# Optimization experiments

Measured on AMD Instinct MI355X. Metric: run time of the kernel, lower is better.

The kernel has to match this reference:

```python
import jax, jax.numpy as jnp
import numpy as np

B, T, E = 4, 2048, 2048
H, HKV, HD = 16, 8, 128
THETA = 10000.0
SCALE_BASE = 512.0


def _rotate_half(x):
    x1, x2 = jnp.split(x, 2, axis=-1)
    return jnp.concatenate([-x2, x1], axis=-1)


def _xpos_tables(seqlen):
    # cos/sin/scale tables for XPos rotary, all [seqlen, HD], fp32 compute dtype
    half_idx = jnp.arange(0, HD, 2, dtype=jnp.float32)
    inv_freq = 1.0 / (THETA ** (half_idx / HD))            # [HD/2]
    t = jnp.arange(seqlen, dtype=jnp.float32)
    freqs = jnp.outer(t, inv_freq)                          # [seqlen, HD/2]
    emb = jnp.concatenate([freqs, freqs], axis=-1)          # [seqlen, HD]
    cos, sin = jnp.cos(emb), jnp.sin(emb)
    # xpos decay: ((2i + 0.4d)/(1.4d)) ** ((t - L/2)/scale_base)
    scale_vec = (half_idx + 0.4 * HD) / (1.4 * HD)          # [HD/2]
    power = (t - seqlen // 2) / SCALE_BASE                  # [seqlen]
    scale = scale_vec[None, :] ** power[:, None]            # [seqlen, HD/2]
    scale = jnp.concatenate([scale, scale], axis=-1)        # [seqlen, HD]
    return cos, sin, scale


def setup_inputs() -> dict:
    key = jax.random.key(0)
    ks = jax.random.split(key, 5)
    std = 0.02
    return {
        "x": jax.random.normal(ks[0], (B, T, E), dtype=jnp.float32),
        "W_q": jax.random.normal(ks[1], (E, H * HD), dtype=jnp.float32) * std,
        "W_k": jax.random.normal(ks[2], (E, HKV * HD), dtype=jnp.float32) * std,
        "W_v": jax.random.normal(ks[3], (E, HKV * HD), dtype=jnp.float32) * std,
        "W_o": jax.random.normal(ks[4], (E, E), dtype=jnp.float32) * std,
    }


def reference(x, W_q, W_k, W_v, W_o):
    b, t, _ = x.shape
    q = (x @ W_q).reshape(b, t, H, HD)       # [B,T,H,HD]
    k = (x @ W_k).reshape(b, t, HKV, HD)     # [B,T,HKV,HD]
    v = (x @ W_v).reshape(b, t, HKV, HD)
    rep = H // HKV                            # GQA: repeat_interleave over head dim
    k = jnp.repeat(k, rep, axis=2)
    v = jnp.repeat(v, rep, axis=2)

    cos, sin, scale = _xpos_tables(t)         # past_len = 0 (no kv cache)
    cos = cos[None, :, None, :]
    sin = sin[None, :, None, :]
    scale = scale[None, :, None, :]
    q = q * scale
    q = q * cos + _rotate_half(q) * sin
    k = k / scale
    k = k * cos + _rotate_half(k) * sin

    inv_sqrt_d = 1.0 / jnp.sqrt(jnp.float32(HD))
    scores = jnp.einsum('bqhd,bkhd->bhqk', q, k) * inv_sqrt_d  # [B,H,T,T]
    causal = jnp.triu(jnp.ones((t, t), dtype=bool), k=1)
    scores = jnp.where(causal[None, None], -jnp.inf, scores)
    probs = jax.nn.softmax(scores, axis=-1)
    attn = jnp.einsum('bhqk,bkhd->bqhd', probs, v)             # [B,T,H,HD]
    out = attn.reshape(b, t, E) @ W_o
    return out
```

## Files before the change

### kernel.cpp

```cpp
#include <hip/hip_runtime.h>

typedef _Float16 f16;
typedef __attribute__((ext_vector_type(8))) _Float16 f16x8;
typedef __attribute__((ext_vector_type(4))) _Float16 f16x4;
typedef __attribute__((ext_vector_type(4))) float f32x4;
typedef __attribute__((ext_vector_type(16))) float f32x16;
typedef __attribute__((ext_vector_type(4))) unsigned u32x4;

#define T_SEQ 2048
#define NBATCH 4

__device__ __forceinline__ void gld_lds16(const f16* g, f16* l) {
    __builtin_amdgcn_global_load_lds((const __attribute__((address_space(1))) void*)g,
                                     (__attribute__((address_space(3))) void*)l, 16, 0, 0);
}

__device__ __forceinline__ unsigned pk2(float a, float b) {
    __attribute__((ext_vector_type(2))) __fp16 h = __builtin_amdgcn_cvt_pkrtz(a, b);
    return __builtin_bit_cast(unsigned, h);
}

__global__ __launch_bounds__(256) void k_cast(const float* __restrict__ in,
                                              f16* __restrict__ out, int n4) {
    int i = blockIdx.x * 256 + threadIdx.x;
    if (i < n4) {
        float4 v = ((const float4*)in)[i];
        f16x4 o = { (f16)v.x, (f16)v.y, (f16)v.z, (f16)v.w };
        ((f16x4*)out)[i] = o;
    }
}

__global__ __launch_bounds__(256) void k_transpose(const float* __restrict__ src,
                                                   f16* __restrict__ dst, int K, int N) {
    __shared__ float tile[32][33];
    int n0 = blockIdx.x * 32, k0 = blockIdx.y * 32;
    int tx = threadIdx.x & 31, ty = threadIdx.x >> 5;
#pragma unroll
    for (int j = 0; j < 32; j += 8)
        tile[ty + j][tx] = src[(size_t)(k0 + ty + j) * N + n0 + tx];
    __syncthreads();
#pragma unroll
    for (int j = 0; j < 32; j += 8)
        dst[(size_t)(n0 + ty + j) * K + k0 + tx] = (f16)tile[tx][ty + j];
}

__global__ __launch_bounds__(256) void k_tables(float* __restrict__ tab) {
    int i = blockIdx.x * 256 + threadIdx.x;
    int t = i >> 6, f = i & 63;
    float inv_freq = powf(10000.0f, -(2.0f * f) / 128.0f);
    float ang = (float)t * inv_freq;
    float sv = (2.0f * f + 51.2f) / 179.2f;
    float pw = ((float)t - 1024.0f) / 512.0f;
    tab[i] = cosf(ang);
    tab[131072 + i] = sinf(ang);
    tab[262144 + i] = powf(sv, pw);
}

__global__ __launch_bounds__(256) void k_vtrans(const f16* __restrict__ qkv, f16* __restrict__ vtg) {
    const int kt = blockIdx.x, bk = blockIdx.y;
    const int b = bk >> 3, kvh = bk & 7;
    const int tid = threadIdx.x;
    __shared__ f16 tile[64][132];
#pragma unroll
    for (int p = 0; p < 4; ++p) {
        int idx = p * 256 + tid;
        int r = idx >> 4, dc = (idx & 15) * 8;
        f16x8 v = *(const f16x8*)(qkv + (size_t)(b * T_SEQ + kt * 64 + r) * 4096 + 3072 + kvh * 128 + dc);
#pragma unroll
        for (int j = 0; j < 8; ++j) tile[r][dc + j] = v[j];
    }
    __syncthreads();
    f16* outb = vtg + (size_t)(bk * 32 + kt) * 8192;
#pragma unroll
    for (int p = 0; p < 4; ++p) {
        int c = p * 256 + tid;
        int kchunk = c >> 7, d = c & 127;
        f16x8 o;
#pragma unroll
        for (int j = 0; j < 8; ++j) o[j] = tile[kchunk * 8 + j][d];
        *(f16x8*)(outb + (size_t)c * 8) = o;
    }
}

template <typename OutT>
__global__ __launch_bounds__(512, 1) void k_gemm256(const f16* __restrict__ A,
                                                    const f16* __restrict__ B,
                                                    OutT* __restrict__ C, int M, int N, int K) {
    extern __shared__ char smem[];
    f16* As = (f16*)smem;
    f16* Bs = (f16*)smem + 32768;
    const int tid = threadIdx.x, lane = tid & 63, w = tid >> 6;
    const int wr4 = w >> 1, wc2 = w & 1;
    const int cq = lane & 15, gq = lane >> 4;
    const int nbx = gridDim.x;
    const int nwg = nbx * gridDim.y;
    const int bid0 = blockIdx.y * nbx + blockIdx.x;
    const int bid = (bid0 & 7) * (nwg >> 3) + (bid0 >> 3);
    const int m0 = (bid / nbx) * 256, n0 = (bid % nbx) * 256;
    const int KT = K >> 6;

    f32x4 acc[2][2][2][4] = {};
    f16x8 aL[2][2], aH[2][2], bL[4][2], bH[4][2];

    auto stageA = [&](int buf, int half, int t) {
#pragma unroll
        for (int r = 0; r < 2; ++r) {
            int cb = r * 512 + w * 64;
            int c = cb + lane;
            int row = c >> 3, cc = c & 7;
            gld_lds16(A + (size_t)(m0 + half * 128 + row) * K + t * 64 + ((cc ^ (row & 7)) * 8),
                      As + buf * 16384 + half * 8192 + cb * 8);
        }
    };
    auto stageB = [&](int buf, int half, int t) {
#pragma unroll
        for (int r = 0; r < 2; ++r) {
            int cb = r * 512 + w * 64;
            int c = cb + lane;
            int row = c >> 3, cc = c & 7;
            gld_lds16(B + (size_t)(n0 + half * 128 + row) * K + t * 64 + ((cc ^ (row & 7)) * 8),
                      Bs + buf * 16384 + half * 8192 + cb * 8);
        }
    };
    auto rdA = [&](int buf, int qr, f16x8 a[2][2]) {
#pragma unroll
        for (int mi = 0; mi < 2; ++mi)
#pragma unroll
            for (int ks = 0; ks < 2; ++ks) {
                int R = qr * 128 + wr4 * 32 + mi * 16 + cq;
                a[mi][ks] = *(const f16x8*)&As[buf * 16384 + R * 64 + (((ks * 4 + gq) ^ (cq & 7)) * 8)];
            }
    };
    auto rdB = [&](int buf, int qc, f16x8 b[4][2]) {
#pragma unroll
        for (int ni = 0; ni < 4; ++ni)
#pragma unroll
            for (int ks = 0; ks < 2; ++ks) {
                int R = qc * 128 + wc2 * 64 + ni * 16 + cq;
                b[ni][ks] = *(const f16x8*)&Bs[buf * 16384 + R * 64 + (((ks * 4 + gq) ^ (cq & 7)) * 8)];
            }
    };

    stageA(0, 0, 0); stageB(0, 0, 0); stageB(0, 1, 0); stageA(0, 1, 0);
    if (KT > 1) { stageA(1, 0, 1); stageB(1, 0, 1); stageB(1, 1, 1); }
    asm volatile("s_waitcnt vmcnt(6)");
    __builtin_amdgcn_s_barrier();

#pragma unroll 1
    for (int t = 0; t < KT; ++t) {
        const int buf = t & 1;
        rdA(buf, 0, aL); rdB(buf, 0, bL);
        if (t + 1 < KT) stageA(buf ^ 1, 1, t + 1);
        __builtin_amdgcn_s_barrier();
        asm volatile("s_waitcnt lgkmcnt(0)");
        __builtin_amdgcn_sched_barrier(0);
        __builtin_amdgcn_s_setprio(1);
#pragma unroll
        for (int mi = 0; mi < 2; ++mi)
#pragma unroll
            for (int ni = 0; ni < 4; ++ni)
#pragma unroll
                for (int ks = 0; ks < 2; ++ks)
                    acc[0][0][mi][ni] = __builtin_amdgcn_mfma_f32_16x16x32_f16(aL[mi][ks], bL[ni][ks], acc[0][0][mi][ni], 0, 0, 0);
        __builtin_amdgcn_s_setprio(0);
        __builtin_amdgcn_s_barrier();
        rdB(buf, 1, bH);
        if (t + 2 < KT) stageA(buf, 0, t + 2);
        __builtin_amdgcn_s_barrier();
        asm volatile("s_waitcnt lgkmcnt(0)");
        __builtin_amdgcn_sched_barrier(0);
        __builtin_amdgcn_s_setprio(1);
#pragma unroll
        for (int mi = 0; mi < 2; ++mi)
#pragma unroll
            for (int ni = 0; ni < 4; ++ni)
#pragma unroll
                for (int ks = 0; ks < 2; ++ks)
                    acc[0][1][mi][ni] = __builtin_amdgcn_mfma_f32_16x16x32_f16(aL[mi][ks], bH[ni][ks], acc[0][1][mi][ni], 0, 0, 0);
        __builtin_amdgcn_s_setprio(0);
        __builtin_amdgcn_s_barrier();
        rdA(buf, 1, aH);
        if (t + 2 < KT) stageB(buf, 0, t + 2);
        __builtin_amdgcn_s_barrier();
        asm volatile("s_waitcnt lgkmcnt(0)");
        __builtin_amdgcn_sched_barrier(0);
        __builtin_amdgcn_s_setprio(1);
#pragma unroll
        for (int mi = 0; mi < 2; ++mi)
#pragma unroll
            for (int ni = 0; ni < 4; ++ni)
#pragma unroll
                for (int ks = 0; ks < 2; ++ks)
                    acc[1][1][mi][ni] = __builtin_amdgcn_mfma_f32_16x16x32_f16(aH[mi][ks], bH[ni][ks], acc[1][1][mi][ni], 0, 0, 0);
        __builtin_amdgcn_s_setprio(0);
        __builtin_amdgcn_s_barrier();
        if (t + 2 < KT) stageB(buf, 1, t + 2);
        __builtin_amdgcn_s_barrier();
        __builtin_amdgcn_sched_barrier(0);
        __builtin_amdgcn_s_setprio(1);
#pragma unroll
        for (int mi = 0; mi < 2; ++mi)
#pragma unroll
            for (int ni = 0; ni < 4; ++ni)
#pragma unroll
                for (int ks = 0; ks < 2; ++ks)
                    acc[1][0][mi][ni] = __builtin_amdgcn_mfma_f32_16x16x32_f16(aH[mi][ks], bL[ni][ks], acc[1][0][mi][ni], 0, 0, 0);
        __builtin_amdgcn_s_setprio(0);
        if (t + 2 < KT) asm volatile("s_waitcnt vmcnt(6)");
        else            asm volatile("s_waitcnt vmcnt(0)");
        __builtin_amdgcn_s_barrier();
    }

#pragma unroll
    for (int qr = 0; qr < 2; ++qr)
#pragma unroll
        for (int qc = 0; qc < 2; ++qc)
#pragma unroll
            for (int mi = 0; mi < 2; ++mi)
#pragma unroll
                for (int ni = 0; ni < 4; ++ni)
#pragma unroll
                    for (int i = 0; i < 4; ++i) {
                        int row = m0 + qr * 128 + wr4 * 32 + mi * 16 + gq * 4 + i;
                        int col = n0 + qc * 128 + wc2 * 64 + ni * 16 + cq;
                        C[(size_t)row * N + col] = (OutT)acc[qr][qc][mi][ni][i];
                    }
}

__global__ __launch_bounds__(256) void k_rope(f16* __restrict__ qkv, const float* __restrict__ tab) {
    int idx = blockIdx.x * 256 + threadIdx.x;
    const int QTOT = NBATCH * T_SEQ * 16 * 64;
    int f, col0, bt;
    bool isQ = idx < QTOT;
    if (isQ) {
        f = idx & 63; int hh = (idx >> 6) & 15; bt = idx >> 10;
        col0 = hh * 128 + f;
    } else {
        int j = idx - QTOT;
        f = j & 63; int hh = (j >> 6) & 7; bt = j >> 9;
        col0 = 2048 + hh * 128 + f;
    }
    int t = bt & (T_SEQ - 1);
    float cs = tab[t * 64 + f], sn = tab[131072 + t * 64 + f], sc = tab[262144 + t * 64 + f];
    float mult = isQ ? sc * 0.08838834764831845f : 1.0f / sc;
    size_t p = (size_t)bt * 4096 + col0;
    float x1 = (float)qkv[p], x2 = (float)qkv[p + 64];
    qkv[p]      = (f16)((x1 * cs - x2 * sn) * mult);
    qkv[p + 64] = (f16)((x2 * cs + x1 * sn) * mult);
}

__global__ __launch_bounds__(256) void k_attn(const f16* __restrict__ qkv,
                                              const f16* __restrict__ vtg,
                                              f16* __restrict__ ao) {
    const int bid0 = blockIdx.x;
    const int bid = (bid0 & 7) * 64 + (bid0 >> 3);
    const int pr = bid & 7, h = (bid >> 3) & 15, b = bid >> 7;
    const int kvh = h >> 1, bk = b * 8 + kvh;
    const int tid = threadIdx.x, lane = tid & 63, w = tid >> 6;
    const int l31 = lane & 31, hi = lane >> 5;

    __shared__ f16 Klds[2][64 * 128];
    __shared__ f16 Vlds[2][8 * 128 * 8];

    const f16* kbase = qkv + (size_t)b * T_SEQ * 4096 + 2048 + kvh * 128;
    const f16* vbase = vtg + (size_t)bk * 32 * 8192;

    auto stage = [&](int buf, int kt) {
#pragma unroll
        for (int qq = 0; qq < 4; ++qq) {
            int c = w * 256 + qq * 64 + lane;
            int row = c >> 4;
            int ch = (c & 15) ^ (row & 15);
            gld_lds16(kbase + (size_t)(kt * 64 + row) * 4096 + ch * 8,
                      &Klds[buf][(w * 256 + qq * 64) * 8]);
        }
#pragma unroll
        for (int qq = 0; qq < 4; ++qq) {
            int c = w * 256 + qq * 64 + lane;
            gld_lds16(vbase + ((size_t)kt * 1024 + c) * 8,
                      &Vlds[buf][(w * 256 + qq * 64) * 8]);
        }
    };

#pragma unroll 1
    for (int hf = 0; hf < 2; ++hf) {
        const int qt = hf ? pr : (15 - pr);
        const int q0 = qt * 128;
        const int nkt = 2 * qt + 2;
        const int qrow = q0 + w * 32 + l31;

        f16x8 qf[8];
#pragma unroll
        for (int ds = 0; ds < 8; ++ds)
            qf[ds] = *(const f16x8*)(qkv + (size_t)(b * T_SEQ + qrow) * 4096 + h * 128 + ds * 16 + hi * 8);

        f32x16 Ot[4] = {};
        float mrow = -1e30f, lrow = 0.0f;

        stage(0, 0);
        __syncthreads();

#pragma unroll 1
        for (int kt = 0; kt < nkt; ++kt) {
            const int kb = kt & 1;
            if (kt + 1 < nkt) stage(kb ^ 1, kt + 1);

            if (!(kt == 2 * qt + 1 && w < 2)) {
                f32x16 St0 = {}, St1 = {};
                __builtin_amdgcn_s_setprio(1);
#pragma unroll
                for (int ds = 0; ds < 8; ++ds) {
                    int slot = (((2 * ds + hi) ^ (l31 & 15)) << 3);
                    f16x8 k0 = *(const f16x8*)&Klds[kb][l31 * 128 + slot];
                    f16x8 k1 = *(const f16x8*)&Klds[kb][(32 + l31) * 128 + slot];
                    St0 = __builtin_amdgcn_mfma_f32_32x32x16_f16(k0, qf[ds], St0, 0, 0, 0);
                    St1 = __builtin_amdgcn_mfma_f32_32x32x16_f16(k1, qf[ds], St1, 0, 0, 0);
                }
                __builtin_amdgcn_s_setprio(0);

                if (kt >= 2 * qt) {
                    int kbase2 = kt * 64;
#pragma unroll
                    for (int r = 0; r < 16; ++r) {
                        int krel = (r & 3) + 8 * (r >> 2) + 4 * hi;
                        if (kbase2 + krel > qrow) St0[r] = -1e30f;
                        if (kbase2 + 32 + krel > qrow) St1[r] = -1e30f;
                    }
                }

                float tm[16];
#pragma unroll
                for (int r = 0; r < 16; ++r) tm[r] = fmaxf(St0[r], St1[r]);
#pragma unroll
                for (int d = 8; d >= 1; d >>= 1)
#pragma unroll
                    for (int r = 0; r < 8; ++r)
                        if (r < d) tm[r] = fmaxf(tm[r], tm[r + d]);
                float tmax = tm[0];
                float mtile = fmaxf(tmax, __shfl_xor(tmax, 32, 64));

                if (!__all((mtile - mrow) <= 8.0f)) {
                    float mnew = fmaxf(mrow, mtile);
                    float fs = __expf(mrow - mnew);
                    mrow = mnew;
                    lrow *= fs;
#pragma unroll
                    for (int dblk = 0; dblk < 4; ++dblk)
#pragma unroll
                        for (int e = 0; e < 16; ++e) Ot[dblk][e] *= fs;
                }
#pragma unroll
                for (int r = 0; r < 16; ++r) {
                    St0[r] = __expf(St0[r] - mrow);
                    St1[r] = __expf(St1[r] - mrow);
                }
                float ts[16];
#pragma unroll
                for (int r = 0; r < 16; ++r) ts[r] = St0[r] + St1[r];
#pragma unroll
                for (int d = 8; d >= 1; d >>= 1)
#pragma unroll
                    for (int r = 0; r < 8; ++r)
                        if (r < d) ts[r] += ts[r + d];
                float tsum = ts[0];
                lrow += tsum + __shfl_xor(tsum, 32, 64);

#define PV_P(o, pos) ((o) < 4 ? St0[((o) & 3) * 4 + (pos)] : St1[((o) & 3) * 4 + (pos)])
#pragma unroll
                for (int s = 0; s < 4; ++s) {
                    unsigned x1 = pk2(PV_P(2 * s, 0), PV_P(2 * s, 1));
                    unsigned x2 = pk2(PV_P(2 * s, 2), PV_P(2 * s, 3));
                    unsigned y1 = pk2(PV_P(2 * s + 1, 0), PV_P(2 * s + 1, 1));
                    unsigned y2 = pk2(PV_P(2 * s + 1, 2), PV_P(2 * s + 1, 3));
                    unsigned sx1 = __shfl_xor(x1, 32, 64);
                    unsigned sx2 = __shfl_xor(x2, 32, 64);
                    unsigned sy1 = __shfl_xor(y1, 32, 64);
                    unsigned sy2 = __shfl_xor(y2, 32, 64);
                    u32x4 pw;
                    pw[0] = hi ? sy1 : x1;
                    pw[1] = hi ? sy2 : x2;
                    pw[2] = hi ? y1 : sx1;
                    pw[3] = hi ? y2 : sx2;
                    f16x8 pa = __builtin_bit_cast(f16x8, pw);
                    __builtin_amdgcn_s_setprio(1);
#pragma unroll
                    for (int dblk = 0; dblk < 4; ++dblk) {
                        f16x8 vb = *(const f16x8*)&Vlds[kb][(((2 * s + hi) << 7) + 32 * dblk + l31) << 3];
                        Ot[dblk] = __builtin_amdgcn_mfma_f32_32x32x16_f16(vb, pa, Ot[dblk], 0, 0, 0);
                    }
                    __builtin_amdgcn_s_setprio(0);
                }
#undef PV_P
            }
            __syncthreads();
        }

        {
            float inv = 1.0f / lrow;
            size_t rowb = (size_t)(b * T_SEQ + qrow) * 2048 + h * 128;
#pragma unroll
            for (int dblk = 0; dblk < 4; ++dblk)
#pragma unroll
                for (int rg = 0; rg < 4; ++rg) {
                    f16x4 o4 = { (f16)(Ot[dblk][rg * 4 + 0] * inv), (f16)(Ot[dblk][rg * 4 + 1] * inv),
                                 (f16)(Ot[dblk][rg * 4 + 2] * inv), (f16)(Ot[dblk][rg * 4 + 3] * inv) };
                    *(f16x4*)(ao + rowb + dblk * 32 + rg * 8 + hi * 4) = o4;
                }
        }
    }
}

extern "C" void kernel_launch(void* const* d_in, const int* in_sizes, int n_in,
                              void* d_out, int out_size, void* d_ws, size_t ws_size,
                              hipStream_t stream) {
    const float* x  = (const float*)d_in[0];
    const float* Wq = (const float*)d_in[1];
    const float* Wk = (const float*)d_in[2];
    const float* Wv = (const float*)d_in[3];
    const float* Wo = (const float*)d_in[4];
    float* out = (float*)d_out;

    f16* xh    = (f16*)d_ws;
    f16* wqkvT = xh + (size_t)16777216;
    f16* woT   = wqkvT + (size_t)8388608;
    f16* qkv   = woT + (size_t)4194304;
    float* tab = (float*)(qkv + (size_t)33554432);
    f16* ao  = xh;
    f16* vtg = wqkvT;

    hipFuncSetAttribute(reinterpret_cast<const void*>(&k_gemm256<f16>),
                        hipFuncAttributeMaxDynamicSharedMemorySize, 131072);
    hipFuncSetAttribute(reinterpret_cast<const void*>(&k_gemm256<float>),
                        hipFuncAttributeMaxDynamicSharedMemorySize, 131072);

    k_cast<<<16384, 256, 0, stream>>>(x, xh, 4194304);
    k_transpose<<<dim3(64, 64), 256, 0, stream>>>(Wq, wqkvT, 2048, 2048);
    k_transpose<<<dim3(32, 64), 256, 0, stream>>>(Wk, wqkvT + (size_t)2048 * 2048, 2048, 1024);
    k_transpose<<<dim3(32, 64), 256, 0, stream>>>(Wv, wqkvT + (size_t)3072 * 2048, 2048, 1024);
    k_transpose<<<dim3(64, 64), 256, 0, stream>>>(Wo, woT, 2048, 2048);
    k_tables<<<512, 256, 0, stream>>>(tab);
    k_gemm256<f16><<<dim3(16, 32), 512, 131072, stream>>>(xh, wqkvT, qkv, 8192, 4096, 2048);
    k_vtrans<<<dim3(32, 32), 256, 0, stream>>>(qkv, vtg);
    k_rope<<<49152, 256, 0, stream>>>(qkv, tab);
    k_attn<<<512, 256, 0, stream>>>(qkv, vtg, ao);
    k_gemm256<float><<<dim3(8, 32), 512, 131072, stream>>>(ao, woT, out, 8192, 2048, 2048);
}
```

Measured before the change: 453.5 us.

## Share K/V tiles across GQA head pair in attention and merge prep kernels

The attention kernel now uses 512-thread blocks in which two groups of four waves handle the two query heads that share one KV head. Each K/V tile is staged into LDS once per pair, which halves global K/V traffic and the per-wave staging work. Separately, the cast, four weight transposes and table generation are merged into a single prep launch to cut launch overhead. Larger blocks reduce the grid to 256 blocks and may lower occupancy or worsen load balance on the causal schedule.

```diff
diff --git a/kernel.cpp b/kernel.cpp
--- a/kernel.cpp
+++ b/kernel.cpp
@@ -20,20 +20,43 @@
     return __builtin_bit_cast(unsigned, h);
 }
 
-__global__ __launch_bounds__(256) void k_cast(const float* __restrict__ in,
-                                              f16* __restrict__ out, int n4) {
-    int i = blockIdx.x * 256 + threadIdx.x;
-    if (i < n4) {
-        float4 v = ((const float4*)in)[i];
+__global__ __launch_bounds__(256) void k_prep(const float* __restrict__ x,
+                                              const float* __restrict__ Wq,
+                                              const float* __restrict__ Wk,
+                                              const float* __restrict__ Wv,
+                                              const float* __restrict__ Wo,
+                                              f16* __restrict__ xh,
+                                              f16* __restrict__ wqkvT,
+                                              f16* __restrict__ woT,
+                                              float* __restrict__ tab) {
+    __shared__ float tile[32][33];
+    int bidx = blockIdx.x;
+    if (bidx < 16384) {
+        int i = bidx * 256 + threadIdx.x;
+        float4 v = ((const float4*)x)[i];
         f16x4 o = { (f16)v.x, (f16)v.y, (f16)v.z, (f16)v.w };
-        ((f16x4*)out)[i] = o;
-    }
-}
-
-__global__ __launch_bounds__(256) void k_transpose(const float* __restrict__ src,
-                                                   f16* __restrict__ dst, int K, int N) {
-    __shared__ float tile[32][33];
-    int n0 = blockIdx.x * 32, k0 = blockIdx.y * 32;
+        ((f16x4*)xh)[i] = o;
+        return;
+    }
+    bidx -= 16384;
+    if (bidx >= 12288) {
+        int i = (bidx - 12288) * 256 + threadIdx.x;
+        int t = i >> 6, f = i & 63;
+        float inv_freq = powf(10000.0f, -(2.0f * f) / 128.0f);
+        float ang = (float)t * inv_freq;
+        float sv = (2.0f * f + 51.2f) / 179.2f;
+        float pw = ((float)t - 1024.0f) / 512.0f;
+        tab[i] = cosf(ang);
+        tab[131072 + i] = sinf(ang);
+        tab[262144 + i] = powf(sv, pw);
+        return;
+    }
+    const float* src; f16* dst; int N, bx, by;
+    if (bidx < 4096)      { src = Wq; dst = wqkvT;                      N = 2048; bx = bidx & 63; by = bidx >> 6; }
+    else if (bidx < 6144) { src = Wk; dst = wqkvT + (size_t)2048 * 2048; N = 1024; int t2 = bidx - 4096; bx = t2 & 31; by = t2 >> 5; }
+    else if (bidx < 8192) { src = Wv; dst = wqkvT + (size_t)3072 * 2048; N = 1024; int t2 = bidx - 6144; bx = t2 & 31; by = t2 >> 5; }
+    else                  { src = Wo; dst = woT;                        N = 2048; int t2 = bidx - 8192; bx = t2 & 63; by = t2 >> 6; }
+    int n0 = bx * 32, k0 = by * 32;
     int tx = threadIdx.x & 31, ty = threadIdx.x >> 5;
 #pragma unroll
     for (int j = 0; j < 32; j += 8)
@@ -41,19 +64,7 @@
     __syncthreads();
 #pragma unroll
     for (int j = 0; j < 32; j += 8)
-        dst[(size_t)(n0 + ty + j) * K + k0 + tx] = (f16)tile[tx][ty + j];
-}
-
-__global__ __launch_bounds__(256) void k_tables(float* __restrict__ tab) {
-    int i = blockIdx.x * 256 + threadIdx.x;
-    int t = i >> 6, f = i & 63;
-    float inv_freq = powf(10000.0f, -(2.0f * f) / 128.0f);
-    float ang = (float)t * inv_freq;
-    float sv = (2.0f * f + 51.2f) / 179.2f;
-    float pw = ((float)t - 1024.0f) / 512.0f;
-    tab[i] = cosf(ang);
-    tab[131072 + i] = sinf(ang);
-    tab[262144 + i] = powf(sv, pw);
+        dst[(size_t)(n0 + ty + j) * 2048 + k0 + tx] = (f16)tile[tx][ty + j];
 }
 
 __global__ __launch_bounds__(256) void k_vtrans(const f16* __restrict__ qkv, f16* __restrict__ vtg) {
@@ -249,14 +260,16 @@
     qkv[p + 64] = (f16)((x2 * cs + x1 * sn) * mult);
 }
 
-__global__ __launch_bounds__(256) void k_attn(const f16* __restrict__ qkv,
+__global__ __launch_bounds__(512) void k_attn(const f16* __restrict__ qkv,
                                               const f16* __restrict__ vtg,
                                               f16* __restrict__ ao) {
     const int bid0 = blockIdx.x;
-    const int bid = (bid0 & 7) * 64 + (bid0 >> 3);
-    const int pr = bid & 7, h = (bid >> 3) & 15, b = bid >> 7;
-    const int kvh = h >> 1, bk = b * 8 + kvh;
+    const int bid = (bid0 & 7) * 32 + (bid0 >> 3);
+    const int pr = bid & 7, kvh = (bid >> 3) & 7, b = bid >> 6;
+    const int bk = b * 8 + kvh;
     const int tid = threadIdx.x, lane = tid & 63, w = tid >> 6;
+    const int w4 = w & 3, hg = w >> 2;
+    const int h = kvh * 2 + hg;
     const int l31 = lane & 31, hi = lane >> 5;
 
     __shared__ f16 Klds[2][64 * 128];
@@ -267,18 +280,18 @@
 
     auto stage = [&](int buf, int kt) {
 #pragma unroll
-        for (int qq = 0; qq < 4; ++qq) {
-            int c = w * 256 + qq * 64 + lane;
+        for (int qq = 0; qq < 2; ++qq) {
+            int c = w * 128 + qq * 64 + lane;
             int row = c >> 4;
             int ch = (c & 15) ^ (row & 15);
             gld_lds16(kbase + (size_t)(kt * 64 + row) * 4096 + ch * 8,
-                      &Klds[buf][(w * 256 + qq * 64) * 8]);
-        }
-#pragma unroll
-        for (int qq = 0; qq < 4; ++qq) {
-            int c = w * 256 + qq * 64 + lane;
+                      &Klds[buf][(w * 128 + qq * 64) * 8]);
+        }
+#pragma unroll
+        for (int qq = 0; qq < 2; ++qq) {
+            int c = w * 128 + qq * 64 + lane;
             gld_lds16(vbase + ((size_t)kt * 1024 + c) * 8,
-                      &Vlds[buf][(w * 256 + qq * 64) * 8]);
+                      &Vlds[buf][(w * 128 + qq * 64) * 8]);
         }
     };
 
@@ -287,7 +300,7 @@
         const int qt = hf ? pr : (15 - pr);
         const int q0 = qt * 128;
         const int nkt = 2 * qt + 2;
-        const int qrow = q0 + w * 32 + l31;
+        const int qrow = q0 + w4 * 32 + l31;
 
         f16x8 qf[8];
 #pragma unroll
@@ -305,7 +318,7 @@
             const int kb = kt & 1;
             if (kt + 1 < nkt) stage(kb ^ 1, kt + 1);
 
-            if (!(kt == 2 * qt + 1 && w < 2)) {
+            if (!(kt == 2 * qt + 1 && w4 < 2)) {
                 f32x16 St0 = {}, St1 = {};
                 __builtin_amdgcn_s_setprio(1);
 #pragma unroll
@@ -433,15 +446,10 @@
     hipFuncSetAttribute(reinterpret_cast<const void*>(&k_gemm256<float>),
                         hipFuncAttributeMaxDynamicSharedMemorySize, 131072);
 
-    k_cast<<<16384, 256, 0, stream>>>(x, xh, 4194304);
-    k_transpose<<<dim3(64, 64), 256, 0, stream>>>(Wq, wqkvT, 2048, 2048);
-    k_transpose<<<dim3(32, 64), 256, 0, stream>>>(Wk, wqkvT + (size_t)2048 * 2048, 2048, 1024);
-    k_transpose<<<dim3(32, 64), 256, 0, stream>>>(Wv, wqkvT + (size_t)3072 * 2048, 2048, 1024);
-    k_transpose<<<dim3(64, 64), 256, 0, stream>>>(Wo, woT, 2048, 2048);
-    k_tables<<<512, 256, 0, stream>>>(tab);
+    k_prep<<<29184, 256, 0, stream>>>(x, Wq, Wk, Wv, Wo, xh, wqkvT, woT, tab);
     k_gemm256<f16><<<dim3(16, 32), 512, 131072, stream>>>(xh, wqkvT, qkv, 8192, 4096, 2048);
     k_vtrans<<<dim3(32, 32), 256, 0, stream>>>(qkv, vtg);
     k_rope<<<49152, 256, 0, stream>>>(qkv, tab);
-    k_attn<<<512, 256, 0, stream>>>(qkv, vtg, ao);
+    k_attn<<<256, 512, 0, stream>>>(qkv, vtg, ao);
     k_gemm256<float><<<dim3(8, 32), 512, 131072, stream>>>(ao, woT, out, 8192, 2048, 2048);
 }
```

Result: faster. 383.2 us (-15.5%).
